# Performance work log

Hardware: AMD Instinct MI355X
Metric: run time of the kernel (lower is better)

## Reference

```python
import jax, jax.numpy as jnp
import numpy as np

B, F, T, D, S = 8, 256, 512, 40, 4


def setup_inputs() -> dict:
    key = jax.random.key(0)
    k1, k2 = jax.random.split(key)
    embeddings = jax.random.normal(k1, (B, F, T, D), dtype=jnp.float32)
    assignments = jax.random.uniform(k2, (B, F, T, S), dtype=jnp.float32)
    return {"embeddings": embeddings, "assignments": assignments}


def reference(embeddings, assignments):
    b, f, t, d = embeddings.shape
    s = assignments.shape[-1]
    n = f * t
    E = embeddings.reshape(b, n, d)          # (B, N, D)
    V = assignments.reshape(b, n, s)         # (B, N, S)
    # ||VV^T - EE^T||_F^2 summed over batch, via trace identity:
    #   = ||V^T V||_F^2 - 2 ||V^T E||_F^2 + ||E^T E||_F^2
    VtV = jnp.einsum('bns,bnt->bst', V, V)   # (B, S, S)
    VtE = jnp.einsum('bns,bnd->bsd', V, E)   # (B, S, D)
    EtE = jnp.einsum('bnd,bne->bde', E, E)   # (B, D, D)
    fro_sq = jnp.sum(VtV * VtV) - 2.0 * jnp.sum(VtE * VtE) + jnp.sum(EtE * EtE)
    return fro_sq / (b * n)
```

## Files before the change

### kernel.cpp

```cpp
#include <hip/hip_runtime.h>
#include <hip/hip_bf16.h>

#define BATCHES 8
#define NROWS (256 * 512)
#define DE 40
#define SV 4
#define GP 48
#define GSZ (GP * GP)
#define ROWS_PER_BLOCK 1024
#define CHUNKS (NROWS / ROWS_PER_BLOCK)
#define RSTAGE 128
#define NSTAGES (ROWS_PER_BLOCK / RSTAGE)
#define COLBYTES 256
#define TILEBYTES (GP * COLBYTES)

typedef __attribute__((ext_vector_type(8))) short bf16x8;
typedef __attribute__((ext_vector_type(4))) float f32x4;
typedef __attribute__((ext_vector_type(2))) int i32x2;

__device__ __forceinline__ int pk_bf16(float lo, float hi) {
    __hip_bfloat162 h2 = __float22bfloat162_rn(float2{lo, hi});
    return *reinterpret_cast<int*>(&h2);
}

struct ARegs { float4 a0, a1, a2, a3; };

__global__ __launch_bounds__(256, 4) void gram_kernel(const float* __restrict__ E,
                                                      const float* __restrict__ V,
                                                      float* __restrict__ P) {
    __shared__ __align__(16) char tb[2][TILEBYTES];
    __shared__ float gsum[GSZ];

    const int tid = threadIdx.x;
    const int lane = tid & 63;
    const int wave = tid >> 6;
    const int b = blockIdx.x / CHUNKS;
    const int chunk = blockIdx.x % CHUNKS;
    const size_t row0 = (size_t)chunk * ROWS_PER_BLOCK;

    const float4* __restrict__ Eg = (const float4*)(E + (size_t)b * NROWS * DE) + row0 * 10;
    const float4* __restrict__ Vg = (const float4*)(V + (size_t)b * NROWS * SV) + row0;

    for (int i = tid; i < GSZ; i += 256) gsum[i] = 0.f;
    if (tid < 128) {
        const int bb = tid >> 6, off = (tid & 63) * 16;
        *(float4*)&tb[bb][44 * COLBYTES + off] = make_float4(0.f, 0.f, 0.f, 0.f);
    }

    const int cgA = tid % 11, rgA = tid / 11;
    const int cgB = (tid + 256) % 11, rgB = (tid + 256) / 11;
    const bool hasB = (tid < 96);
    const bool vA = (cgA == 10), vB = (cgB == 10);
    const int pA = vA ? 1 : 10, cA = vA ? 0 : cgA;
    const int pB = vB ? 1 : 10, cB = vB ? 0 : cgB;
    const float4* __restrict__ gA = vA ? Vg : Eg;
    const float4* __restrict__ gB = vB ? Vg : Eg;
    const int oA = 4 * rgA * pA + cA;
    const int oB = 4 * rgB * pB + cB;

    f32x4 acc[6];
    #pragma unroll
    for (int i = 0; i < 6; ++i) acc[i] = (f32x4){0.f, 0.f, 0.f, 0.f};

    const int fcol = lane & 15;
    const int fq = lane >> 4;
    const int foff = ((wave * 64 + fq * 16) + 16 * fcol) & 255;

    ARegs A[2];
    float4 b0, b1, b2, b3;

    auto load_a = [&](ARegs& r, int sidx) {
        const int adv = sidx * RSTAGE;
        r.a0 = gA[oA + adv * pA];          r.a1 = gA[oA + adv * pA + pA];
        r.a2 = gA[oA + adv * pA + 2 * pA]; r.a3 = gA[oA + adv * pA + 3 * pA];
    };
    auto load_b = [&](int sidx) {
        if (!hasB) return;
        const int adv = sidx * RSTAGE;
        b0 = gB[oB + adv * pB];          b1 = gB[oB + adv * pB + pB];
        b2 = gB[oB + adv * pB + 2 * pB]; b3 = gB[oB + adv * pB + 3 * pB];
    };
    auto write_stage = [&](const ARegs& r, int bufidx) {
        char* base = tb[bufidx];
        #pragma unroll
        for (int j = 0; j < 4; ++j) {
            const float f0 = (j == 0) ? r.a0.x : (j == 1) ? r.a0.y : (j == 2) ? r.a0.z : r.a0.w;
            const float f1 = (j == 0) ? r.a1.x : (j == 1) ? r.a1.y : (j == 2) ? r.a1.z : r.a1.w;
            const float f2 = (j == 0) ? r.a2.x : (j == 1) ? r.a2.y : (j == 2) ? r.a2.z : r.a2.w;
            const float f3 = (j == 0) ? r.a3.x : (j == 1) ? r.a3.y : (j == 2) ? r.a3.z : r.a3.w;
            const int col = 4 * cgA + j;
            const int off = (8 * rgA + 16 * (col & 15)) & 255;
            i32x2 p = { pk_bf16(f0, f1), pk_bf16(f2, f3) };
            *(i32x2*)&base[col * COLBYTES + off] = p;
        }
        if (hasB) {
            #pragma unroll
            for (int j = 0; j < 4; ++j) {
                const float f0 = (j == 0) ? b0.x : (j == 1) ? b0.y : (j == 2) ? b0.z : b0.w;
                const float f1 = (j == 0) ? b1.x : (j == 1) ? b1.y : (j == 2) ? b1.z : b1.w;
                const float f2 = (j == 0) ? b2.x : (j == 1) ? b2.y : (j == 2) ? b2.z : b2.w;
                const float f3 = (j == 0) ? b3.x : (j == 1) ? b3.y : (j == 2) ? b3.z : b3.w;
                const int col = 4 * cgB + j;
                const int off = (8 * rgB + 16 * (col & 15)) & 255;
                i32x2 p = { pk_bf16(f0, f1), pk_bf16(f2, f3) };
                *(i32x2*)&base[col * COLBYTES + off] = p;
            }
        }
    };

    load_a(A[0], 0);
    load_b(0);
    write_stage(A[0], 0);
    load_a(A[1], 1);
    load_b(1);
    load_a(A[0], 2);
    __syncthreads();

    for (int s = 0; s < NSTAGES; ++s) {
        {
            const char* base = tb[s & 1];
            const bf16x8 f0 = *(const bf16x8*)&base[(0 * 16 + fcol) * COLBYTES + foff];
            const bf16x8 f1 = *(const bf16x8*)&base[(1 * 16 + fcol) * COLBYTES + foff];
            const bf16x8 f2 = *(const bf16x8*)&base[(2 * 16 + fcol) * COLBYTES + foff];
            acc[0] = __builtin_amdgcn_mfma_f32_16x16x32_bf16(f0, f0, acc[0], 0, 0, 0);
            acc[1] = __builtin_amdgcn_mfma_f32_16x16x32_bf16(f1, f0, acc[1], 0, 0, 0);
            acc[2] = __builtin_amdgcn_mfma_f32_16x16x32_bf16(f1, f1, acc[2], 0, 0, 0);
            acc[3] = __builtin_amdgcn_mfma_f32_16x16x32_bf16(f2, f0, acc[3], 0, 0, 0);
            acc[4] = __builtin_amdgcn_mfma_f32_16x16x32_bf16(f2, f1, acc[4], 0, 0, 0);
            acc[5] = __builtin_amdgcn_mfma_f32_16x16x32_bf16(f2, f2, acc[5], 0, 0, 0);
        }
        if (s + 1 < NSTAGES) write_stage(A[(s + 1) & 1], (s + 1) & 1);
        if (s + 3 < NSTAGES) load_a(A[(s + 1) & 1], s + 3);
        if (s + 2 < NSTAGES) load_b(s + 2);
        __syncthreads();
    }

    #pragma unroll
    for (int w = 0; w < 4; ++w) {
        if (wave == w) {
            #pragma unroll
            for (int t6 = 0; t6 < 6; ++t6) {
                const int t = (t6 < 1) ? 0 : (t6 < 3) ? 1 : 2;
                const int u = (t6 == 0) ? 0 : (t6 < 3) ? (t6 - 1) : (t6 - 3);
                #pragma unroll
                for (int r = 0; r < 4; ++r) {
                    const int gi = 16 * t + 4 * fq + r;
                    const int gj = 16 * u + fcol;
                    gsum[gi * GP + gj] += acc[t6][r];
                }
            }
        }
        __syncthreads();
    }

    const float4* gs4 = (const float4*)gsum;
    float4* P4 = (float4*)(P + (size_t)blockIdx.x * GSZ);
    for (int i = tid; i < GSZ / 4; i += 256) P4[i] = gs4[i];
}

__global__ __launch_bounds__(256) void reduce_finish(const float* __restrict__ P,
                                                     float* __restrict__ out) {
    const int tid = threadIdx.x;
    const int b = blockIdx.x / 36;
    const int e0 = (blockIdx.x % 36) * 64;
    const int cs = tid / 64;
    const int el = tid % 64;
    const int e = e0 + el;

    float g = 0.f;
    const float* base = P + (size_t)b * CHUNKS * GSZ + e;
    #pragma unroll 4
    for (int c = cs; c < CHUNKS; c += 4) g += base[(size_t)c * GSZ];

    __shared__ float part[4][64];
    part[cs][el] = g;
    __syncthreads();

    float contrib = 0.f;
    if (tid < 64) {
        g = part[0][el] + part[1][el] + part[2][el] + part[3][el];
        const int gi = e / GP, gj = e % GP;
        if (gi < (DE + SV) && gj <= gi) {
            const float w = (gi == gj) ? 1.f : 2.f;
            const float sgn = ((gi < DE) == (gj < DE)) ? 1.f : -1.f;
            contrib = w * sgn * g * g;
        }
        #pragma unroll
        for (int o = 32; o > 0; o >>= 1) contrib += __shfl_down(contrib, o, 64);
        if (tid == 0)
            atomicAdd(out, contrib * (1.f / ((float)BATCHES * (float)NROWS)));
    }
}

extern "C" void kernel_launch(void* const* d_in, const int* in_sizes, int n_in,
                              void* d_out, int out_size, void* d_ws, size_t ws_size,
                              hipStream_t stream) {
    const float* E = (const float*)d_in[0];
    const float* V = (const float*)d_in[1];
    float* P = (float*)d_ws;

    hipMemsetAsync(d_out, 0, sizeof(float), stream);
    gram_kernel<<<BATCHES * CHUNKS, 256, 0, stream>>>(E, V, P);
    reduce_finish<<<BATCHES * 36, 256, 0, stream>>>(P, (float*)d_out);
}
```

Before: 255.9 us.

## Swizzle LDS layout, use nontemporal loads, lighter barriers, and parallel epilogue reduction

Global loads of the embedding and assignment streams now use nontemporal hints, and one prefetch is moved earlier in the prologue. The LDS column swizzle is changed for both the bf16 staging writes and the fragment reads, which aims to cut bank conflicts. __syncthreads is replaced by an LDS-only wait plus a raw barrier, so outstanding global loads are not drained at each stage. The serialized per-wave accumulation into shared gsum is replaced by each wave dumping its partials to LDS, followed by a parallel sum that writes the full padded tile. This also frees the separate gsum shared array, which may allow higher occupancy.

```diff
diff --git a/kernel.cpp b/kernel.cpp
--- a/kernel.cpp
+++ b/kernel.cpp
@@ -17,10 +17,22 @@
 typedef __attribute__((ext_vector_type(8))) short bf16x8;
 typedef __attribute__((ext_vector_type(4))) float f32x4;
 typedef __attribute__((ext_vector_type(2))) int i32x2;
+typedef __attribute__((ext_vector_type(4))) float f4v;
 
 __device__ __forceinline__ int pk_bf16(float lo, float hi) {
     __hip_bfloat162 h2 = __float22bfloat162_rn(float2{lo, hi});
     return *reinterpret_cast<int*>(&h2);
+}
+
+__device__ __forceinline__ float4 ldnt(const float4* p) {
+    f4v v = __builtin_nontemporal_load(reinterpret_cast<const f4v*>(p));
+    return make_float4(v.x, v.y, v.z, v.w);
+}
+
+__device__ __forceinline__ void bar_lgkm() {
+    asm volatile("s_waitcnt lgkmcnt(0)" ::: "memory");
+    __builtin_amdgcn_s_barrier();
+    asm volatile("" ::: "memory");
 }
 
 struct ARegs { float4 a0, a1, a2, a3; };
@@ -29,7 +41,6 @@
                                                       const float* __restrict__ V,
                                                       float* __restrict__ P) {
     __shared__ __align__(16) char tb[2][TILEBYTES];
-    __shared__ float gsum[GSZ];
 
     const int tid = threadIdx.x;
     const int lane = tid & 63;
@@ -41,7 +52,6 @@
     const float4* __restrict__ Eg = (const float4*)(E + (size_t)b * NROWS * DE) + row0 * 10;
     const float4* __restrict__ Vg = (const float4*)(V + (size_t)b * NROWS * SV) + row0;
 
-    for (int i = tid; i < GSZ; i += 256) gsum[i] = 0.f;
     if (tid < 128) {
         const int bb = tid >> 6, off = (tid & 63) * 16;
         *(float4*)&tb[bb][44 * COLBYTES + off] = make_float4(0.f, 0.f, 0.f, 0.f);
@@ -64,21 +74,23 @@
 
     const int fcol = lane & 15;
     const int fq = lane >> 4;
-    const int foff = ((wave * 64 + fq * 16) + 16 * fcol) & 255;
+    const int fo0 = (wave * 64 + fq * 16 + 16 * ((0 + fcol + (fcol >> 2)) & 15)) & 255;
+    const int fo1 = (wave * 64 + fq * 16 + 16 * ((4 + fcol + (fcol >> 2)) & 15)) & 255;
+    const int fo2 = (wave * 64 + fq * 16 + 16 * ((8 + fcol + (fcol >> 2)) & 15)) & 255;
 
     ARegs A[2];
     float4 b0, b1, b2, b3;
 
     auto load_a = [&](ARegs& r, int sidx) {
         const int adv = sidx * RSTAGE;
-        r.a0 = gA[oA + adv * pA];          r.a1 = gA[oA + adv * pA + pA];
-        r.a2 = gA[oA + adv * pA + 2 * pA]; r.a3 = gA[oA + adv * pA + 3 * pA];
+        r.a0 = ldnt(&gA[oA + adv * pA]);          r.a1 = ldnt(&gA[oA + adv * pA + pA]);
+        r.a2 = ldnt(&gA[oA + adv * pA + 2 * pA]); r.a3 = ldnt(&gA[oA + adv * pA + 3 * pA]);
     };
     auto load_b = [&](int sidx) {
         if (!hasB) return;
         const int adv = sidx * RSTAGE;
-        b0 = gB[oB + adv * pB];          b1 = gB[oB + adv * pB + pB];
-        b2 = gB[oB + adv * pB + 2 * pB]; b3 = gB[oB + adv * pB + 3 * pB];
+        b0 = ldnt(&gB[oB + adv * pB]);          b1 = ldnt(&gB[oB + adv * pB + pB]);
+        b2 = ldnt(&gB[oB + adv * pB + 2 * pB]); b3 = ldnt(&gB[oB + adv * pB + 3 * pB]);
     };
     auto write_stage = [&](const ARegs& r, int bufidx) {
         char* base = tb[bufidx];
@@ -89,7 +101,7 @@
             const float f2 = (j == 0) ? r.a2.x : (j == 1) ? r.a2.y : (j == 2) ? r.a2.z : r.a2.w;
             const float f3 = (j == 0) ? r.a3.x : (j == 1) ? r.a3.y : (j == 2) ? r.a3.z : r.a3.w;
             const int col = 4 * cgA + j;
-            const int off = (8 * rgA + 16 * (col & 15)) & 255;
+            const int off = (8 * rgA + 16 * ((5 * cgA + j) & 15)) & 255;
             i32x2 p = { pk_bf16(f0, f1), pk_bf16(f2, f3) };
             *(i32x2*)&base[col * COLBYTES + off] = p;
         }
@@ -101,7 +113,7 @@
                 const float f2 = (j == 0) ? b2.x : (j == 1) ? b2.y : (j == 2) ? b2.z : b2.w;
                 const float f3 = (j == 0) ? b3.x : (j == 1) ? b3.y : (j == 2) ? b3.z : b3.w;
                 const int col = 4 * cgB + j;
-                const int off = (8 * rgB + 16 * (col & 15)) & 255;
+                const int off = (8 * rgB + 16 * ((5 * cgB + j) & 15)) & 255;
                 i32x2 p = { pk_bf16(f0, f1), pk_bf16(f2, f3) };
                 *(i32x2*)&base[col * COLBYTES + off] = p;
             }
@@ -110,18 +122,18 @@
 
     load_a(A[0], 0);
     load_b(0);
+    load_a(A[1], 1);
     write_stage(A[0], 0);
-    load_a(A[1], 1);
     load_b(1);
     load_a(A[0], 2);
-    __syncthreads();
+    bar_lgkm();
 
     for (int s = 0; s < NSTAGES; ++s) {
         {
             const char* base = tb[s & 1];
-            const bf16x8 f0 = *(const bf16x8*)&base[(0 * 16 + fcol) * COLBYTES + foff];
-            const bf16x8 f1 = *(const bf16x8*)&base[(1 * 16 + fcol) * COLBYTES + foff];
-            const bf16x8 f2 = *(const bf16x8*)&base[(2 * 16 + fcol) * COLBYTES + foff];
+            const bf16x8 f0 = *(const bf16x8*)&base[(0 * 16 + fcol) * COLBYTES + fo0];
+            const bf16x8 f1 = *(const bf16x8*)&base[(1 * 16 + fcol) * COLBYTES + fo1];
+            const bf16x8 f2 = *(const bf16x8*)&base[(2 * 16 + fcol) * COLBYTES + fo2];
             acc[0] = __builtin_amdgcn_mfma_f32_16x16x32_bf16(f0, f0, acc[0], 0, 0, 0);
             acc[1] = __builtin_amdgcn_mfma_f32_16x16x32_bf16(f1, f0, acc[1], 0, 0, 0);
             acc[2] = __builtin_amdgcn_mfma_f32_16x16x32_bf16(f1, f1, acc[2], 0, 0, 0);
@@ -132,30 +144,33 @@
         if (s + 1 < NSTAGES) write_stage(A[(s + 1) & 1], (s + 1) & 1);
         if (s + 3 < NSTAGES) load_a(A[(s + 1) & 1], s + 3);
         if (s + 2 < NSTAGES) load_b(s + 2);
-        __syncthreads();
-    }
-
+        bar_lgkm();
+    }
+
+    float* part = (float*)tb;
     #pragma unroll
-    for (int w = 0; w < 4; ++w) {
-        if (wave == w) {
-            #pragma unroll
-            for (int t6 = 0; t6 < 6; ++t6) {
-                const int t = (t6 < 1) ? 0 : (t6 < 3) ? 1 : 2;
-                const int u = (t6 == 0) ? 0 : (t6 < 3) ? (t6 - 1) : (t6 - 3);
-                #pragma unroll
-                for (int r = 0; r < 4; ++r) {
-                    const int gi = 16 * t + 4 * fq + r;
-                    const int gj = 16 * u + fcol;
-                    gsum[gi * GP + gj] += acc[t6][r];
-                }
-            }
-        }
-        __syncthreads();
-    }
-
-    const float4* gs4 = (const float4*)gsum;
-    float4* P4 = (float4*)(P + (size_t)blockIdx.x * GSZ);
-    for (int i = tid; i < GSZ / 4; i += 256) P4[i] = gs4[i];
+    for (int t6 = 0; t6 < 6; ++t6) {
+        #pragma unroll
+        for (int r = 0; r < 4; ++r)
+            part[((wave * 6 + t6) * 16 + fq * 4 + r) * 16 + fcol] = acc[t6][r];
+    }
+    bar_lgkm();
+
+    float* __restrict__ Pb = P + (size_t)blockIdx.x * GSZ;
+    #pragma unroll
+    for (int i = 0; i < 9; ++i) {
+        const int e = tid + 256 * i;
+        const unsigned gi = (unsigned)e / GP, gj = (unsigned)e % GP;
+        const int t = gi >> 4, u = gj >> 4;
+        float v = 0.f;
+        if (u <= t) {
+            const int t6 = (t * (t + 1) / 2) + u;
+            const int idx = (t6 * 16 + (gi & 15)) * 16 + (gj & 15);
+            v = part[0 * 1536 + idx] + part[1 * 1536 + idx]
+              + part[2 * 1536 + idx] + part[3 * 1536 + idx];
+        }
+        Pb[e] = v;
+    }
 }
 
 __global__ __launch_bounds__(256) void reduce_finish(const float* __restrict__ P,
@@ -199,7 +214,7 @@
     const float* V = (const float*)d_in[1];
     float* P = (float*)d_ws;
 
-    hipMemsetAsync(d_out, 0, sizeof(float), stream);
+    (void)hipMemsetAsync(d_out, 0, sizeof(float), stream);
     gram_kernel<<<BATCHES * CHUNKS, 256, 0, stream>>>(E, V, P);
     reduce_finish<<<BATCHES * 36, 256, 0, stream>>>(P, (float*)d_out);
 }
```

Result: faster. 242.0 us (-5.5%).
